# Performance work log

Measured on AMD Instinct MI355X. Metric: run time of the kernel, lower is better.

Reference implementation:

```python
import jax, jax.numpy as jnp
import numpy as np

B, T, D = 2, 2048, 512
H, L, DFF, W = 8, 4, 2048, 256
DH = D // H  # 64
EPS = 1e-5


def layer_norm(x, g, b):
    mu = jnp.mean(x, axis=-1, keepdims=True)
    var = jnp.var(x, axis=-1, keepdims=True)
    return (x - mu) * jax.lax.rsqrt(var + EPS) * g + b


def setup_inputs() -> dict:
    key = jax.random.key(0)
    ks = jax.random.split(key, 8)
    s = 0.02
    inp = {
        "tokens": jax.random.normal(ks[0], (B, T, D), jnp.float32),
        "Wq": jax.random.normal(ks[1], (L, D, D), jnp.float32) * s,
        "Wk": jax.random.normal(ks[2], (L, D, D), jnp.float32) * s,
        "Wv": jax.random.normal(ks[3], (L, D, D), jnp.float32) * s,
        "Wo": jax.random.normal(ks[4], (L, D, D), jnp.float32) * s,
        "bq": jnp.zeros((L, D), jnp.float32),
        "bk": jnp.zeros((L, D), jnp.float32),
        "bv": jnp.zeros((L, D), jnp.float32),
        "bo": jnp.zeros((L, D), jnp.float32),
        "W1": jax.random.normal(ks[5], (L, D, DFF), jnp.float32) * s,
        "b1": jnp.zeros((L, DFF), jnp.float32),
        "W2": jax.random.normal(ks[6], (L, DFF, D), jnp.float32) * s,
        "b2": jnp.zeros((L, D), jnp.float32),
        "g1": jnp.ones((L, D), jnp.float32),
        "be1": jnp.zeros((L, D), jnp.float32),
        "g2": jnp.ones((L, D), jnp.float32),
        "be2": jnp.zeros((L, D), jnp.float32),
        "gf": jnp.ones((D,), jnp.float32),
        "bf": jnp.zeros((D,), jnp.float32),
    }
    return inp


def _rope_tables():
    pos = jnp.arange(T, dtype=jnp.float32)  # default position_ids = 0..T-1
    inv_freq = 1.0 / (10000.0 ** (jnp.arange(0, DH, 2, dtype=jnp.float32) / DH))
    ang = pos[:, None] * inv_freq[None, :]            # (T, DH/2)
    cos = jnp.concatenate([jnp.cos(ang), jnp.cos(ang)], axis=-1)  # (T, DH)
    sin = jnp.concatenate([jnp.sin(ang), jnp.sin(ang)], axis=-1)
    return cos, sin


def _rotate_half(x):
    return jnp.concatenate([-x[..., DH // 2:], x[..., :DH // 2]], axis=-1)


def reference(tokens, Wq, Wk, Wv, Wo, bq, bk, bv, bo, W1, b1, W2, b2,
              g1, be1, g2, be2, gf, bf):
    cos, sin = _rope_tables()  # (T, DH) each, broadcast over (B,H,T,DH)
    # sliding-window causal mask: allow j<=i and i-j < W
    idx = jnp.arange(T)
    allow = (idx[None, :] <= idx[:, None]) & ((idx[:, None] - idx[None, :]) < W)
    scale = np.sqrt(DH).astype(np.float32)

    x = tokens
    for l in range(L):
        xn = layer_norm(x, g1[l], be1[l])
        q = (xn @ Wq[l] + bq[l]).reshape(B, T, H, DH).transpose(0, 2, 1, 3)
        k = (xn @ Wk[l] + bk[l]).reshape(B, T, H, DH).transpose(0, 2, 1, 3)
        v = (xn @ Wv[l] + bv[l]).reshape(B, T, H, DH).transpose(0, 2, 1, 3)
        q = q * cos + _rotate_half(q) * sin
        k = k * cos + _rotate_half(k) * sin
        scores = jnp.einsum('bhqd,bhkd->bhqk', q, k) / scale
        scores = jnp.where(allow[None, None], scores, -jnp.inf)
        attn = jax.nn.softmax(scores, axis=-1)
        out = jnp.einsum('bhqk,bhkd->bhqd', attn, v)
        out = out.transpose(0, 2, 1, 3).reshape(B, T, D)
        x = x + out @ Wo[l] + bo[l]
        xn2 = layer_norm(x, g2[l], be2[l])
        h = jax.nn.gelu(xn2 @ W1[l] + b1[l], approximate=False)  # torch GELU = exact erf
        x = x + h @ W2[l] + b2[l]
    return layer_norm(x, gf, bf)
```

## Files before the change

kernel.cpp:

```cpp
#include <hip/hip_runtime.h>
#include <hip/hip_bf16.h>

#define BQ 2
#define TT 2048
#define DD 512
#define HH 8
#define LL 4
#define DFFN 2048
#define WWIN 256
#define DHD 64
#define MM (BQ*TT)
#define NOUT (MM*DD)

typedef __attribute__((ext_vector_type(8))) short bf16x8;
typedef __attribute__((ext_vector_type(4))) float f32x4;

__device__ __forceinline__ void lds_load16(const void* g, void* l) {
  __builtin_amdgcn_global_load_lds((const __attribute__((address_space(1))) void*)g,
                                   (__attribute__((address_space(3))) void*)l,
                                   16, 0, 0);
}

__global__ __launch_bounds__(256) void fill_const(float* __restrict__ out, float C, int n) {
  int i = blockIdx.x * 256 + threadIdx.x;
  if (i < n) out[i] = C;
}

__global__ __launch_bounds__(256) void prep(const float* __restrict__ tokens,
                                            float* __restrict__ x,
                                            const float* __restrict__ bq,
                                            const float* __restrict__ bk,
                                            const float* __restrict__ bv,
                                            float* __restrict__ bqkvc) {
  const int b = blockIdx.x;
  if (b < 8192) {
    int i = b * 256 + threadIdx.x;
    x[i] = tokens[i];
  } else {
    int idx = (b - 8192) * 256 + threadIdx.x;
    if (idx < LL * 1536) {
      int l = idx / 1536, n = idx % 1536;
      float v;
      if (n < 512)       v = bq[l * 512 + n];
      else if (n < 1024) v = bk[l * 512 + n - 512];
      else               v = bv[l * 512 + n - 1024];
      bqkvc[idx] = v;
    }
  }
}

__global__ __launch_bounds__(256) void transpose_all(const float* __restrict__ Wq,
                                                     const float* __restrict__ Wk,
                                                     const float* __restrict__ Wv,
                                                     const float* __restrict__ Wo,
                                                     const float* __restrict__ W1,
                                                     const float* __restrict__ W2,
                                                     __hip_bfloat16* __restrict__ wqkvT,
                                                     __hip_bfloat16* __restrict__ woT,
                                                     __hip_bfloat16* __restrict__ w1T,
                                                     __hip_bfloat16* __restrict__ w2T) {
  __shared__ float tile[32][33];
  const int l = blockIdx.y;
  const int b = blockIdx.x;
  const float* src;
  __hip_bfloat16* dst;
  int K, N, t;
  if (b < 768) {
    int which = b >> 8; t = b & 255;
    src = ((which == 0) ? Wq : (which == 1) ? Wk : Wv) + (size_t)l * 262144;
    dst = wqkvT + (size_t)l * 786432 + which * 262144;
    K = 512; N = 512;
  } else if (b < 1024) {
    t = b - 768;  src = Wo + (size_t)l * 262144;  dst = woT + (size_t)l * 262144;  K = 512; N = 512;
  } else if (b < 2048) {
    t = b - 1024; src = W1 + (size_t)l * 1048576; dst = w1T + (size_t)l * 1048576; K = 512; N = 2048;
  } else {
    t = b - 2048; src = W2 + (size_t)l * 1048576; dst = w2T + (size_t)l * 1048576; K = 2048; N = 512;
  }
  const int tilesN = N >> 5;
  const int n0 = (t % tilesN) * 32, k0 = (t / tilesN) * 32;
  const int tx = threadIdx.x & 31, ty = threadIdx.x >> 5;
#pragma unroll
  for (int r = 0; r < 32; r += 8)
    tile[ty + r][tx] = src[(size_t)(k0 + ty + r) * N + n0 + tx];
  __syncthreads();
#pragma unroll
  for (int r = 0; r < 32; r += 8)
    dst[(size_t)(n0 + ty + r) * K + k0 + tx] = __float2bfloat16(tile[tx][ty + r]);
}

__global__ __launch_bounds__(256) void ln_kernel(const float* __restrict__ x,
                                                 const float* __restrict__ g,
                                                 const float* __restrict__ b,
                                                 __hip_bfloat16* __restrict__ out) {
  const int wave = threadIdx.x >> 6, lane = threadIdx.x & 63;
  const int row = blockIdx.x * 4 + wave;
  const float* xr = x + (size_t)row * DD;
  float v[8];
  float s = 0.f;
#pragma unroll
  for (int i = 0; i < 8; ++i) { v[i] = xr[lane + i * 64]; s += v[i]; }
#pragma unroll
  for (int off = 32; off; off >>= 1) s += __shfl_xor(s, off);
  float mu = s * (1.f / DD);
  float qs = 0.f;
#pragma unroll
  for (int i = 0; i < 8; ++i) { float d = v[i] - mu; qs += d * d; }
#pragma unroll
  for (int off = 32; off; off >>= 1) qs += __shfl_xor(qs, off);
  float rstd = rsqrtf(qs * (1.f / DD) + 1e-5f);
#pragma unroll
  for (int i = 0; i < 8; ++i) {
    int c = lane + i * 64;
    out[(size_t)row * DD + c] = __float2bfloat16((v[i] - mu) * rstd * g[c] + b[c]);
  }
}

__global__ __launch_bounds__(256) void ln_f32out(const float* __restrict__ x,
                                                 const float* __restrict__ g,
                                                 const float* __restrict__ b,
                                                 float* __restrict__ out) {
  const int wave = threadIdx.x >> 6, lane = threadIdx.x & 63;
  const int row = blockIdx.x * 4 + wave;
  const float* xr = x + (size_t)row * DD;
  float v[8];
  float s = 0.f;
#pragma unroll
  for (int i = 0; i < 8; ++i) { v[i] = xr[lane + i * 64]; s += v[i]; }
#pragma unroll
  for (int off = 32; off; off >>= 1) s += __shfl_xor(s, off);
  float mu = s * (1.f / DD);
  float qs = 0.f;
#pragma unroll
  for (int i = 0; i < 8; ++i) { float d = v[i] - mu; qs += d * d; }
#pragma unroll
  for (int off = 32; off; off >>= 1) qs += __shfl_xor(qs, off);
  float rstd = rsqrtf(qs * (1.f / DD) + 1e-5f);
#pragma unroll
  for (int i = 0; i < 8; ++i) {
    int c = lane + i * 64;
    out[(size_t)row * DD + c] = (v[i] - mu) * rstd * g[c] + b[c];
  }
}

enum { EPI_BF16 = 0, EPI_GELU = 1, EPI_ADDF32 = 2 };

template <int EPI, bool ROPE, int BN>
__global__ __launch_bounds__(256, 1) void gemm_bt(const __hip_bfloat16* __restrict__ A,
                                                  const __hip_bfloat16* __restrict__ BT,
                                                  const float* __restrict__ bias,
                                                  __hip_bfloat16* __restrict__ Obf,
                                                  float* __restrict__ Of,
                                                  __hip_bfloat16* __restrict__ VTo,
                                                  int M, int N, int K, int KS,
                                                  int ostride, int ooff) {
  constexpr int MI = (BN == 128) ? 4 : 2;
  __shared__ __align__(16) __hip_bfloat16 Ash0[128 * 32];
  __shared__ __align__(16) __hip_bfloat16 Ash1[128 * 32];
  __shared__ __align__(16) __hip_bfloat16 Bsh0[BN * 32];
  __shared__ __align__(16) __hip_bfloat16 Bsh1[BN * 32];
  const int tid = threadIdx.x;
  const int wave = tid >> 6;
  const int lane = tid & 63;
  const int m0 = blockIdx.y * 128;
  const int n0 = blockIdx.x * BN;
  const int kbase = blockIdx.z * KS;
  const int wm = (BN == 128) ? (wave >> 1) * 64 : wave * 32;
  const int wn = (BN == 128) ? (wave & 1) * 64 : 0;
  const int l15 = lane & 15;
  const int quad = lane >> 4;

  f32x4 acc[MI][4] = {};

  const int r0 = tid >> 2;
  const int o0 = (tid & 3) * 8;

  const __hip_bfloat16* Ap0 = A + (size_t)(m0 + r0) * K + kbase + o0;
  const __hip_bfloat16* Ap1 = Ap0 + (size_t)64 * K;
  const __hip_bfloat16* Bp0 = BT + (size_t)(n0 + r0) * K + kbase + o0;
  const __hip_bfloat16* Bp1 = Bp0 + (size_t)64 * K;

  auto stage = [&](__hip_bfloat16* As, __hip_bfloat16* Bs, int k) {
    lds_load16(Ap0 + k, As + wave * 512);
    lds_load16(Ap1 + k, As + 2048 + wave * 512);
    lds_load16(Bp0 + k, Bs + wave * 512);
    if constexpr (BN == 128) lds_load16(Bp1 + k, Bs + 2048 + wave * 512);
  };
  auto compute = [&](const __hip_bfloat16* As, const __hip_bfloat16* Bs) {
    bf16x8 af[MI], bfr[4];
#pragma unroll
    for (int i = 0; i < MI; ++i)
      af[i] = *(const bf16x8*)&As[(wm + i * 16 + l15) * 32 + quad * 8];
#pragma unroll
    for (int j = 0; j < 4; ++j)
      bfr[j] = *(const bf16x8*)&Bs[(wn + j * 16 + l15) * 32 + quad * 8];
#pragma unroll
    for (int i = 0; i < MI; ++i)
#pragma unroll
      for (int j = 0; j < 4; ++j)
        acc[i][j] = __builtin_amdgcn_mfma_f32_16x16x32_bf16(af[i], bfr[j], acc[i][j], 0, 0, 0);
  };

  stage(Ash0, Bsh0, 0);
  for (int k0 = 0; k0 < KS; k0 += 64) {
    __syncthreads();
    if (k0 + 32 < KS) stage(Ash1, Bsh1, k0 + 32);
    compute(Ash0, Bsh0);
    __syncthreads();
    if (k0 + 64 < KS) stage(Ash0, Bsh0, k0 + 64);
    compute(Ash1, Bsh1);
  }

  if (ROPE && n0 < 1024) {
#pragma unroll
    for (int j = 0; j < 2; ++j) {
      const int col = n0 + wn + j * 16 + l15;
      const float bv0 = bias[col], bv1 = bias[col + 32];
      const float freq = __powf(10000.f, -(float)(j * 16 + l15) * (1.f / 32.f));
#pragma unroll
      for (int i = 0; i < MI; ++i) {
        const int row = m0 + wm + i * 16 + quad * 4;
#pragma unroll
        for (int r = 0; r < 4; ++r) {
          const int t = (row + r) & 2047;
          float sn, cs;
          __sincosf((float)t * freq, &sn, &cs);
          const float a0 = acc[i][j][r] + bv0;
          const float a1 = acc[i][j + 2][r] + bv1;
          const size_t idx = (size_t)(row + r) * ostride + ooff + col;
          Obf[idx]      = __float2bfloat16(a0 * cs - a1 * sn);
          Obf[idx + 32] = __float2bfloat16(a1 * cs + a0 * sn);
        }
      }
    }
    return;
  }
  if (ROPE) {
#pragma unroll
    for (int j = 0; j < 4; ++j) {
      const int col = n0 + wn + j * 16 + l15;
      const float bv = bias[col];
      const int d = col - 1024;
#pragma unroll
      for (int i = 0; i < MI; ++i) {
        const int row = m0 + wm + i * 16 + quad * 4;
#pragma unroll
        for (int r = 0; r < 4; ++r)
          VTo[(size_t)d * 4096 + row + r] = __float2bfloat16(acc[i][j][r] + bv);
      }
    }
    return;
  }

#pragma unroll
  for (int j = 0; j < 4; ++j) {
    const int col = n0 + wn + j * 16 + l15;
    const float bv = (blockIdx.z == 0) ? bias[col] : 0.f;
#pragma unroll
    for (int i = 0; i < MI; ++i) {
      const int row = m0 + wm + i * 16 + quad * 4;
#pragma unroll
      for (int r = 0; r < 4; ++r) {
        float v = acc[i][j][r] + bv;
        size_t idx = (size_t)(row + r) * ostride + ooff + col;
        if (EPI == EPI_BF16) {
          Obf[idx] = __float2bfloat16(v);
        } else if (EPI == EPI_GELU) {
          float ge = 0.5f * v * (1.f + erff(v * 0.70710678118654752f));
          Obf[idx] = __float2bfloat16(ge);
        } else {
          atomicAdd(&Of[idx], v);
        }
      }
    }
  }
}

__global__ __launch_bounds__(256, 1) void attn_mfma(const __hip_bfloat16* __restrict__ qkv,
                                                    const __hip_bfloat16* __restrict__ VT,
                                                    __hip_bfloat16* __restrict__ ao) {
  constexpr int KPAD = 72;
  constexpr int PPAD = 40;
  __shared__ __align__(16) __hip_bfloat16 Ksh[320 * KPAD];
  __shared__ __align__(16) __hip_bfloat16 Psh[4 * 16 * PPAD];
  const int tid = threadIdx.x;
  const int wave = tid >> 6;
  const int lane = tid & 63;
  const int l15 = lane & 15;
  const int quad = lane >> 4;
  const int bh = blockIdx.y;
  const int b = bh >> 3, h = bh & 7;
  const int q0 = blockIdx.x * 64;
  const int j0 = (q0 >= WWIN) ? (q0 - WWIN) : 0;
  const int nk = (q0 + 63) - j0 + 1;

  const size_t baseK = ((size_t)(b * TT + j0)) * 1536 + 512 + h * 64;
  for (int c = tid; c < nk * 8; c += 256) {
    int row = c >> 3, cc = (c & 7) * 8;
    *(uint4*)&Ksh[row * KPAD + cc] = *(const uint4*)&qkv[baseK + (size_t)row * 1536 + cc];
  }
  __syncthreads();

  const int qt0 = q0 + wave * 16;
  const size_t baseQ = ((size_t)(b * TT + qt0 + l15)) * 1536 + h * 64;
  const bf16x8 aq0 = *(const bf16x8*)&qkv[baseQ + quad * 8];
  const bf16x8 aq1 = *(const bf16x8*)&qkv[baseQ + 32 + quad * 8];

  const __hip_bfloat16* V0 = VT + (size_t)(h * 64 + l15) * 4096 + (size_t)b * 2048 + j0;

  f32x4 o0 = {}, o1 = {}, o2 = {}, o3 = {};
  float lsum[4] = {0.f, 0.f, 0.f, 0.f};

  const int klo = (qt0 > (WWIN - 1)) ? (qt0 - (WWIN - 1)) : 0;
  const int c_lo = (klo - j0) >> 5;
  const int c_hi = (qt0 + 15 - j0) >> 5;
  __hip_bfloat16* Pw = &Psh[wave * 16 * PPAD];

  for (int c = c_lo; c <= c_hi; ++c) {
    const int krel = c * 32;
    bf16x8 bk00 = *(const bf16x8*)&Ksh[(krel + l15) * KPAD + quad * 8];
    bf16x8 bk01 = *(const bf16x8*)&Ksh[(krel + l15) * KPAD + 32 + quad * 8];
    bf16x8 bk10 = *(const bf16x8*)&Ksh[(krel + 16 + l15) * KPAD + quad * 8];
    bf16x8 bk11 = *(const bf16x8*)&Ksh[(krel + 16 + l15) * KPAD + 32 + quad * 8];
    f32x4 z = {};
    f32x4 s0 = __builtin_amdgcn_mfma_f32_16x16x32_bf16(aq0, bk00, z, 0, 0, 0);
    s0 = __builtin_amdgcn_mfma_f32_16x16x32_bf16(aq1, bk01, s0, 0, 0, 0);
    f32x4 s1 = __builtin_amdgcn_mfma_f32_16x16x32_bf16(aq0, bk10, z, 0, 0, 0);
    s1 = __builtin_amdgcn_mfma_f32_16x16x32_bf16(aq1, bk11, s1, 0, 0, 0);

    const int jj0 = j0 + krel + l15;
    const int jj1 = jj0 + 16;
#pragma unroll
    for (int r = 0; r < 4; ++r) {
      const int qrow = qt0 + quad * 4 + r;
      const bool ok0 = (jj0 <= qrow) && ((qrow - jj0) < WWIN);
      const bool ok1 = (jj1 <= qrow) && ((qrow - jj1) < WWIN);
      const float p0 = ok0 ? __expf(s0[r] * 0.125f) : 0.f;
      const float p1 = ok1 ? __expf(s1[r] * 0.125f) : 0.f;
      lsum[r] += p0 + p1;
      const int qloc = quad * 4 + r;
      Pw[qloc * PPAD + l15]      = __float2bfloat16(p0);
      Pw[qloc * PPAD + 16 + l15] = __float2bfloat16(p1);
    }
    asm volatile("s_waitcnt lgkmcnt(0)" ::: "memory");
    __builtin_amdgcn_wave_barrier();
    const bf16x8 pa = *(const bf16x8*)&Pw[l15 * PPAD + quad * 8];

    const int kgl = krel + quad * 8;
#pragma unroll
    for (int t = 0; t < 4; ++t) {
      const bf16x8 bv = *(const bf16x8*)&V0[(size_t)t * 65536 + kgl];
      if (t == 0)      o0 = __builtin_amdgcn_mfma_f32_16x16x32_bf16(pa, bv, o0, 0, 0, 0);
      else if (t == 1) o1 = __builtin_amdgcn_mfma_f32_16x16x32_bf16(pa, bv, o1, 0, 0, 0);
      else if (t == 2) o2 = __builtin_amdgcn_mfma_f32_16x16x32_bf16(pa, bv, o2, 0, 0, 0);
      else             o3 = __builtin_amdgcn_mfma_f32_16x16x32_bf16(pa, bv, o3, 0, 0, 0);
    }
    __builtin_amdgcn_wave_barrier();
  }

#pragma unroll
  for (int r = 0; r < 4; ++r) {
#pragma unroll
    for (int off = 8; off; off >>= 1) lsum[r] += __shfl_xor(lsum[r], off, 16);
  }

#pragma unroll
  for (int r = 0; r < 4; ++r) {
    const float inv = 1.f / lsum[r];
    const size_t ob = ((size_t)(b * TT + qt0 + quad * 4 + r)) * DD + h * 64 + l15;
    ao[ob]      = __float2bfloat16(o0[r] * inv);
    ao[ob + 16] = __float2bfloat16(o1[r] * inv);
    ao[ob + 32] = __float2bfloat16(o2[r] * inv);
    ao[ob + 48] = __float2bfloat16(o3[r] * inv);
  }
}

extern "C" void kernel_launch(void* const* d_in, const int* in_sizes, int n_in,
                              void* d_out, int out_size, void* d_ws, size_t ws_size,
                              hipStream_t stream) {
  float* outF = (float*)d_out;

  int code = 0;
  if (n_in != 19)                      code = 1;
  else if (in_sizes[0]  != 2097152)    code = 2;
  else if (in_sizes[1]  != 1048576)    code = 3;
  else if (in_sizes[9]  != 4194304)    code = 4;
  else if (in_sizes[17] != 512)        code = 5;
  if (code != 0 || ws_size < 27287552ull) {
    float C = code ? (150.f + 15.f * (float)code) : (1000.f + (float)(ws_size >> 20));
    fill_const<<<8192, 256, 0, stream>>>(outF, C, NOUT);
    return;
  }

  const float* tokens = (const float*)d_in[0];
  const float* Wq  = (const float*)d_in[1];
  const float* Wk  = (const float*)d_in[2];
  const float* Wv  = (const float*)d_in[3];
  const float* Wo  = (const float*)d_in[4];
  const float* bq  = (const float*)d_in[5];
  const float* bk  = (const float*)d_in[6];
  const float* bv  = (const float*)d_in[7];
  const float* bo  = (const float*)d_in[8];
  const float* W1  = (const float*)d_in[9];
  const float* b1  = (const float*)d_in[10];
  const float* W2  = (const float*)d_in[11];
  const float* b2  = (const float*)d_in[12];
  const float* g1  = (const float*)d_in[13];
  const float* be1 = (const float*)d_in[14];
  const float* g2  = (const float*)d_in[15];
  const float* be2 = (const float*)d_in[16];
  const float* gf  = (const float*)d_in[17];
  const float* bf  = (const float*)d_in[18];

  char* ws = (char*)d_ws;
  __hip_bfloat16* xnao  = (__hip_bfloat16*)(ws + 0);
  __hip_bfloat16* qkv   = (__hip_bfloat16*)(ws + 4194304);
  __hip_bfloat16* hbuf  = (__hip_bfloat16*)(ws + 4194304);
  __hip_bfloat16* VT    = (__hip_bfloat16*)(ws + 16777216);

  const bool big = ws_size >= 46161920ull;
  __hip_bfloat16 *wqkvT, *woT, *w1T, *w2T;
  float* bqkvc;
  if (big) {
    wqkvT = (__hip_bfloat16*)(ws + 20971520);
    woT   = (__hip_bfloat16*)(ws + 27262976);
    w1T   = (__hip_bfloat16*)(ws + 29360128);
    w2T   = (__hip_bfloat16*)(ws + 37748736);
    bqkvc = (float*)(ws + 46137344);
  } else {
    wqkvT = (__hip_bfloat16*)(ws + 20971520);
    woT   = (__hip_bfloat16*)(ws + 22544384);
    w1T   = (__hip_bfloat16*)(ws + 23068672);
    w2T   = (__hip_bfloat16*)(ws + 25165824);
    bqkvc = (float*)(ws + 27262976);
  }
  __hip_bfloat16* xn = xnao;
  __hip_bfloat16* ao = xnao;
  float* x = outF;

  if (big) {
    transpose_all<<<dim3(3072, 4), 256, 0, stream>>>(Wq, Wk, Wv, Wo, W1, W2,
                                                     wqkvT, woT, w1T, w2T);
  }
  prep<<<8216, 256, 0, stream>>>(tokens, x, bq, bk, bv, bqkvc);

  for (int l = 0; l < LL; ++l) {
    if (!big) {
      transpose_all<<<dim3(3072, 1), 256, 0, stream>>>(
          Wq + (size_t)l * 262144, Wk + (size_t)l * 262144, Wv + (size_t)l * 262144,
          Wo + (size_t)l * 262144, W1 + (size_t)l * 1048576, W2 + (size_t)l * 1048576,
          wqkvT, woT, w1T, w2T);
    }
    __hip_bfloat16* qkvT_l = big ? wqkvT + (size_t)l * 786432  : wqkvT;
    __hip_bfloat16* woT_l  = big ? woT   + (size_t)l * 262144  : woT;
    __hip_bfloat16* w1T_l  = big ? w1T   + (size_t)l * 1048576 : w1T;
    __hip_bfloat16* w2T_l  = big ? w2T   + (size_t)l * 1048576 : w2T;

    ln_kernel<<<1024, 256, 0, stream>>>(x, g1 + l * 512, be1 + l * 512, xn);
    gemm_bt<EPI_BF16, true, 64><<<dim3(24, 32), 256, 0, stream>>>(
        xn, qkvT_l, bqkvc + l * 1536, qkv, nullptr, VT, MM, 1536, 512, 512, 1536, 0);
    attn_mfma<<<dim3(32, 16), 256, 0, stream>>>(qkv, VT, ao);
    gemm_bt<EPI_ADDF32, false, 64><<<dim3(8, 32, 2), 256, 0, stream>>>(
        ao, woT_l, bo + l * 512, nullptr, x, nullptr, MM, 512, 512, 256, 512, 0);
    ln_kernel<<<1024, 256, 0, stream>>>(x, g2 + l * 512, be2 + l * 512, xn);
    gemm_bt<EPI_GELU, false, 128><<<dim3(16, 32), 256, 0, stream>>>(
        xn, w1T_l, b1 + l * 2048, hbuf, nullptr, nullptr, MM, 2048, 512, 512, 2048, 0);
    gemm_bt<EPI_ADDF32, false, 128><<<dim3(4, 32, 4), 256, 0, stream>>>(
        hbuf, w2T_l, b2 + l * 512, nullptr, x, nullptr, MM, 512, 2048, 512, 512, 0);
  }
  ln_f32out<<<1024, 256, 0, stream>>>(x, gf, bf, outF);
}
```

Before: 600.9 us.

## Replace atomic split-K accumulation with partial buffers fused into residual add plus LayerNorm

When the workspace is large enough, the Wo and W2 split-K GEMMs write their two partial results to separate fp32 buffers instead of doing atomicAdd into the residual. A new add_ln2 kernel sums residual plus both partials and applies the next LayerNorm in one pass, producing both the fp32 residual and the bf16 normalized activation. This drops the atomics, the extra copy of tokens and the separate LN launches, at the cost of more workspace and extra fp32 partial traffic.

```diff
diff --git a/kernel.cpp b/kernel.cpp
--- a/kernel.cpp
+++ b/kernel.cpp
@@ -11,6 +11,7 @@
 #define DHD 64
 #define MM (BQ*TT)
 #define NOUT (MM*DD)
+#define PSTRIDE 2097152
 
 typedef __attribute__((ext_vector_type(8))) short bf16x8;
 typedef __attribute__((ext_vector_type(4))) float f32x4;
@@ -47,6 +48,20 @@
       bqkvc[idx] = v;
     }
   }
+}
+
+__global__ __launch_bounds__(256) void prep_bias(const float* __restrict__ bq,
+                                                 const float* __restrict__ bk,
+                                                 const float* __restrict__ bv,
+                                                 float* __restrict__ bqkvc) {
+  int idx = blockIdx.x * 256 + threadIdx.x;
+  if (idx >= LL * 1536) return;
+  int l = idx / 1536, n = idx % 1536;
+  float v;
+  if (n < 512)       v = bq[l * 512 + n];
+  else if (n < 1024) v = bk[l * 512 + n - 512];
+  else               v = bv[l * 512 + n - 1024];
+  bqkvc[idx] = v;
 }
 
 __global__ __launch_bounds__(256) void transpose_all(const float* __restrict__ Wq,
@@ -143,7 +158,70 @@
   }
 }
 
-enum { EPI_BF16 = 0, EPI_GELU = 1, EPI_ADDF32 = 2 };
+template <int OUTMODE>
+__global__ __launch_bounds__(256) void add_ln2(const float* __restrict__ xin,
+                                               const float* __restrict__ P,
+                                               const float* __restrict__ g,
+                                               const float* __restrict__ bsh,
+                                               float* __restrict__ xout,
+                                               __hip_bfloat16* __restrict__ xnout,
+                                               float* __restrict__ fout) {
+  const int wave = threadIdx.x >> 6, lane = threadIdx.x & 63;
+  const int row = blockIdx.x * 4 + wave;
+  const size_t base = (size_t)row * DD + lane * 8;
+  float v[8];
+  {
+    float4 a0 = *(const float4*)&xin[base];
+    float4 a1 = *(const float4*)&xin[base + 4];
+    float4 p0 = *(const float4*)&P[base];
+    float4 p1 = *(const float4*)&P[base + 4];
+    float4 q0 = *(const float4*)&P[PSTRIDE + base];
+    float4 q1 = *(const float4*)&P[PSTRIDE + base + 4];
+    v[0] = a0.x + p0.x + q0.x; v[1] = a0.y + p0.y + q0.y;
+    v[2] = a0.z + p0.z + q0.z; v[3] = a0.w + p0.w + q0.w;
+    v[4] = a1.x + p1.x + q1.x; v[5] = a1.y + p1.y + q1.y;
+    v[6] = a1.z + p1.z + q1.z; v[7] = a1.w + p1.w + q1.w;
+  }
+  float s = 0.f;
+#pragma unroll
+  for (int j = 0; j < 8; ++j) s += v[j];
+#pragma unroll
+  for (int off = 32; off; off >>= 1) s += __shfl_xor(s, off);
+  const float mu = s * (1.f / DD);
+  float qs = 0.f;
+#pragma unroll
+  for (int j = 0; j < 8; ++j) { float d = v[j] - mu; qs += d * d; }
+#pragma unroll
+  for (int off = 32; off; off >>= 1) qs += __shfl_xor(qs, off);
+  const float rstd = rsqrtf(qs * (1.f / DD) + 1e-5f);
+  const int c0 = lane * 8;
+  float4 g0 = *(const float4*)&g[c0];
+  float4 g1 = *(const float4*)&g[c0 + 4];
+  float4 b0 = *(const float4*)&bsh[c0];
+  float4 b1 = *(const float4*)&bsh[c0 + 4];
+  const float gg[8] = {g0.x, g0.y, g0.z, g0.w, g1.x, g1.y, g1.z, g1.w};
+  const float bb[8] = {b0.x, b0.y, b0.z, b0.w, b1.x, b1.y, b1.z, b1.w};
+  if (OUTMODE == 0) {
+    float4 xa = {v[0], v[1], v[2], v[3]};
+    float4 xb = {v[4], v[5], v[6], v[7]};
+    *(float4*)&xout[base] = xa;
+    *(float4*)&xout[base + 4] = xb;
+    bf16x8 o;
+#pragma unroll
+    for (int j = 0; j < 8; ++j)
+      ((__hip_bfloat16*)&o)[j] = __float2bfloat16((v[j] - mu) * rstd * gg[j] + bb[j]);
+    *(bf16x8*)&xnout[base] = o;
+  } else {
+    float4 oa = {(v[0] - mu) * rstd * gg[0] + bb[0], (v[1] - mu) * rstd * gg[1] + bb[1],
+                 (v[2] - mu) * rstd * gg[2] + bb[2], (v[3] - mu) * rstd * gg[3] + bb[3]};
+    float4 ob = {(v[4] - mu) * rstd * gg[4] + bb[4], (v[5] - mu) * rstd * gg[5] + bb[5],
+                 (v[6] - mu) * rstd * gg[6] + bb[6], (v[7] - mu) * rstd * gg[7] + bb[7]};
+    *(float4*)&fout[base] = oa;
+    *(float4*)&fout[base + 4] = ob;
+  }
+}
+
+enum { EPI_BF16 = 0, EPI_GELU = 1, EPI_ADDF32 = 2, EPI_PART = 3 };
 
 template <int EPI, bool ROPE, int BN>
 __global__ __launch_bounds__(256, 1) void gemm_bt(const __hip_bfloat16* __restrict__ A,
@@ -252,6 +330,7 @@
     return;
   }
 
+  const size_t zoff = (EPI == EPI_PART) ? (size_t)blockIdx.z * (size_t)M * N : 0;
 #pragma unroll
   for (int j = 0; j < 4; ++j) {
     const int col = n0 + wn + j * 16 + l15;
@@ -268,6 +347,8 @@
         } else if (EPI == EPI_GELU) {
           float ge = 0.5f * v * (1.f + erff(v * 0.70710678118654752f));
           Obf[idx] = __float2bfloat16(ge);
+        } else if (EPI == EPI_PART) {
+          Of[zoff + idx] = v;
         } else {
           atomicAdd(&Of[idx], v);
         }
@@ -417,16 +498,20 @@
   __hip_bfloat16* qkv   = (__hip_bfloat16*)(ws + 4194304);
   __hip_bfloat16* hbuf  = (__hip_bfloat16*)(ws + 4194304);
   __hip_bfloat16* VT    = (__hip_bfloat16*)(ws + 16777216);
-
-  const bool big = ws_size >= 46161920ull;
+  float* Pwo            = (float*)(ws + 4194304);
+
+  const bool big  = ws_size >= 46161920ull;
+  const bool flow = ws_size >= 62939136ull;
   __hip_bfloat16 *wqkvT, *woT, *w1T, *w2T;
   float* bqkvc;
+  float* Pffn = nullptr;
   if (big) {
     wqkvT = (__hip_bfloat16*)(ws + 20971520);
     woT   = (__hip_bfloat16*)(ws + 27262976);
     w1T   = (__hip_bfloat16*)(ws + 29360128);
     w2T   = (__hip_bfloat16*)(ws + 37748736);
     bqkvc = (float*)(ws + 46137344);
+    Pffn  = (float*)(ws + 46161920);
   } else {
     wqkvT = (__hip_bfloat16*)(ws + 20971520);
     woT   = (__hip_bfloat16*)(ws + 22544384);
@@ -437,6 +522,37 @@
   __hip_bfloat16* xn = xnao;
   __hip_bfloat16* ao = xnao;
   float* x = outF;
+
+  if (flow) {
+    transpose_all<<<dim3(3072, 4), 256, 0, stream>>>(Wq, Wk, Wv, Wo, W1, W2,
+                                                     wqkvT, woT, w1T, w2T);
+    prep_bias<<<24, 256, 0, stream>>>(bq, bk, bv, bqkvc);
+    ln_kernel<<<1024, 256, 0, stream>>>(tokens, g1, be1, xn);
+    for (int l = 0; l < LL; ++l) {
+      __hip_bfloat16* qkvT_l = wqkvT + (size_t)l * 786432;
+      __hip_bfloat16* woT_l  = woT   + (size_t)l * 262144;
+      __hip_bfloat16* w1T_l  = w1T   + (size_t)l * 1048576;
+      __hip_bfloat16* w2T_l  = w2T   + (size_t)l * 1048576;
+
+      gemm_bt<EPI_BF16, true, 64><<<dim3(24, 32), 256, 0, stream>>>(
+          xn, qkvT_l, bqkvc + l * 1536, qkv, nullptr, VT, MM, 1536, 512, 512, 1536, 0);
+      attn_mfma<<<dim3(32, 16), 256, 0, stream>>>(qkv, VT, ao);
+      gemm_bt<EPI_PART, false, 64><<<dim3(8, 32, 2), 256, 0, stream>>>(
+          ao, woT_l, bo + l * 512, nullptr, Pwo, nullptr, MM, 512, 512, 256, 512, 0);
+      add_ln2<0><<<1024, 256, 0, stream>>>(l == 0 ? tokens : x, Pwo,
+                                           g2 + l * 512, be2 + l * 512, x, xn, nullptr);
+      gemm_bt<EPI_GELU, false, 128><<<dim3(16, 32), 256, 0, stream>>>(
+          xn, w1T_l, b1 + l * 2048, hbuf, nullptr, nullptr, MM, 2048, 512, 512, 2048, 0);
+      gemm_bt<EPI_PART, false, 64><<<dim3(8, 32, 2), 256, 0, stream>>>(
+          hbuf, w2T_l, b2 + l * 512, nullptr, Pffn, nullptr, MM, 512, 2048, 1024, 512, 0);
+      if (l < LL - 1)
+        add_ln2<0><<<1024, 256, 0, stream>>>(x, Pffn, g1 + (l + 1) * 512,
+                                             be1 + (l + 1) * 512, x, xn, nullptr);
+      else
+        add_ln2<1><<<1024, 256, 0, stream>>>(x, Pffn, gf, bf, nullptr, nullptr, outF);
+    }
+    return;
+  }
 
   if (big) {
     transpose_all<<<dim3(3072, 4), 256, 0, stream>>>(Wq, Wk, Wv, Wo, W1, W2,
```

Measured after the change: 529.2 us. 11.9% less time.

## Replace split-K atomic residual GEMMs with 64x64 tiles and direct residual epilogue

Applied to the files above, without the earlier changes.

Adds a 64x64 block-tile variant of the GEMM and an epilogue that writes out = residual + acc + bias with plain stores. The Wo and W2 projections now use this variant instead of split-K with float atomics, which removes the atomic traffic while keeping enough blocks to fill the GPU. The token copy in prep is also dropped: the first layer's residual is read straight from tokens, and the first LayerNorm reads tokens directly. The trade-off is that the W2 GEMM now runs its full K=2048 loop in each block with smaller tiles, so each block does more serial work and gets less operand reuse.

```diff
diff --git a/kernel.cpp b/kernel.cpp
--- a/kernel.cpp
+++ b/kernel.cpp
@@ -47,6 +47,20 @@
       bqkvc[idx] = v;
     }
   }
+}
+
+__global__ __launch_bounds__(256) void prep_bias(const float* __restrict__ bq,
+                                                 const float* __restrict__ bk,
+                                                 const float* __restrict__ bv,
+                                                 float* __restrict__ bqkvc) {
+  int idx = blockIdx.x * 256 + threadIdx.x;
+  if (idx >= LL * 1536) return;
+  int l = idx / 1536, n = idx % 1536;
+  float v;
+  if (n < 512)       v = bq[l * 512 + n];
+  else if (n < 1024) v = bk[l * 512 + n - 512];
+  else               v = bv[l * 512 + n - 1024];
+  bqkvc[idx] = v;
 }
 
 __global__ __launch_bounds__(256) void transpose_all(const float* __restrict__ Wq,
@@ -143,34 +157,38 @@
   }
 }
 
-enum { EPI_BF16 = 0, EPI_GELU = 1, EPI_ADDF32 = 2 };
-
-template <int EPI, bool ROPE, int BN>
+enum { EPI_BF16 = 0, EPI_GELU = 1, EPI_ADDF32 = 2, EPI_RES = 3 };
+
+template <int EPI, bool ROPE, int BM, int BN>
 __global__ __launch_bounds__(256, 1) void gemm_bt(const __hip_bfloat16* __restrict__ A,
                                                   const __hip_bfloat16* __restrict__ BT,
                                                   const float* __restrict__ bias,
                                                   __hip_bfloat16* __restrict__ Obf,
                                                   float* __restrict__ Of,
+                                                  const float* __restrict__ Orin,
                                                   __hip_bfloat16* __restrict__ VTo,
                                                   int M, int N, int K, int KS,
                                                   int ostride, int ooff) {
-  constexpr int MI = (BN == 128) ? 4 : 2;
-  __shared__ __align__(16) __hip_bfloat16 Ash0[128 * 32];
-  __shared__ __align__(16) __hip_bfloat16 Ash1[128 * 32];
+  constexpr int MI = (BM == 64) ? 2 : ((BN == 128) ? 4 : 2);
+  constexpr int NJ = (BM == 64) ? 2 : 4;
+  __shared__ __align__(16) __hip_bfloat16 Ash0[BM * 32];
+  __shared__ __align__(16) __hip_bfloat16 Ash1[BM * 32];
   __shared__ __align__(16) __hip_bfloat16 Bsh0[BN * 32];
   __shared__ __align__(16) __hip_bfloat16 Bsh1[BN * 32];
   const int tid = threadIdx.x;
   const int wave = tid >> 6;
   const int lane = tid & 63;
-  const int m0 = blockIdx.y * 128;
+  const int m0 = blockIdx.y * BM;
   const int n0 = blockIdx.x * BN;
   const int kbase = blockIdx.z * KS;
-  const int wm = (BN == 128) ? (wave >> 1) * 64 : wave * 32;
-  const int wn = (BN == 128) ? (wave & 1) * 64 : 0;
+  const int wm = (BM == 64) ? ((wave >> 1) * 32)
+                            : ((BN == 128) ? ((wave >> 1) * 64) : (wave * 32));
+  const int wn = (BM == 64) ? ((wave & 1) * 32)
+                            : ((BN == 128) ? ((wave & 1) * 64) : 0);
   const int l15 = lane & 15;
   const int quad = lane >> 4;
 
-  f32x4 acc[MI][4] = {};
+  f32x4 acc[MI][NJ] = {};
 
   const int r0 = tid >> 2;
   const int o0 = (tid & 3) * 8;
@@ -182,22 +200,22 @@
 
   auto stage = [&](__hip_bfloat16* As, __hip_bfloat16* Bs, int k) {
     lds_load16(Ap0 + k, As + wave * 512);
-    lds_load16(Ap1 + k, As + 2048 + wave * 512);
+    if constexpr (BM == 128) lds_load16(Ap1 + k, As + 2048 + wave * 512);
     lds_load16(Bp0 + k, Bs + wave * 512);
     if constexpr (BN == 128) lds_load16(Bp1 + k, Bs + 2048 + wave * 512);
   };
   auto compute = [&](const __hip_bfloat16* As, const __hip_bfloat16* Bs) {
-    bf16x8 af[MI], bfr[4];
+    bf16x8 af[MI], bfr[NJ];
 #pragma unroll
     for (int i = 0; i < MI; ++i)
       af[i] = *(const bf16x8*)&As[(wm + i * 16 + l15) * 32 + quad * 8];
 #pragma unroll
-    for (int j = 0; j < 4; ++j)
+    for (int j = 0; j < NJ; ++j)
       bfr[j] = *(const bf16x8*)&Bs[(wn + j * 16 + l15) * 32 + quad * 8];
 #pragma unroll
     for (int i = 0; i < MI; ++i)
 #pragma unroll
-      for (int j = 0; j < 4; ++j)
+      for (int j = 0; j < NJ; ++j)
         acc[i][j] = __builtin_amdgcn_mfma_f32_16x16x32_bf16(af[i], bfr[j], acc[i][j], 0, 0, 0);
   };
 
@@ -211,51 +229,51 @@
     compute(Ash1, Bsh1);
   }
 
-  if (ROPE && n0 < 1024) {
-#pragma unroll
-    for (int j = 0; j < 2; ++j) {
-      const int col = n0 + wn + j * 16 + l15;
-      const float bv0 = bias[col], bv1 = bias[col + 32];
-      const float freq = __powf(10000.f, -(float)(j * 16 + l15) * (1.f / 32.f));
-#pragma unroll
-      for (int i = 0; i < MI; ++i) {
-        const int row = m0 + wm + i * 16 + quad * 4;
-#pragma unroll
-        for (int r = 0; r < 4; ++r) {
-          const int t = (row + r) & 2047;
-          float sn, cs;
-          __sincosf((float)t * freq, &sn, &cs);
-          const float a0 = acc[i][j][r] + bv0;
-          const float a1 = acc[i][j + 2][r] + bv1;
-          const size_t idx = (size_t)(row + r) * ostride + ooff + col;
-          Obf[idx]      = __float2bfloat16(a0 * cs - a1 * sn);
-          Obf[idx + 32] = __float2bfloat16(a1 * cs + a0 * sn);
+  if constexpr (ROPE) {
+    if (n0 < 1024) {
+#pragma unroll
+      for (int j = 0; j < 2; ++j) {
+        const int col = n0 + wn + j * 16 + l15;
+        const float bv0 = bias[col], bv1 = bias[col + 32];
+        const float freq = __powf(10000.f, -(float)(j * 16 + l15) * (1.f / 32.f));
+#pragma unroll
+        for (int i = 0; i < MI; ++i) {
+          const int row = m0 + wm + i * 16 + quad * 4;
+#pragma unroll
+          for (int r = 0; r < 4; ++r) {
+            const int t = (row + r) & 2047;
+            float sn, cs;
+            __sincosf((float)t * freq, &sn, &cs);
+            const float a0 = acc[i][j][r] + bv0;
+            const float a1 = acc[i][j + 2][r] + bv1;
+            const size_t idx = (size_t)(row + r) * ostride + ooff + col;
+            Obf[idx]      = __float2bfloat16(a0 * cs - a1 * sn);
+            Obf[idx + 32] = __float2bfloat16(a1 * cs + a0 * sn);
+          }
+        }
+      }
+    } else {
+#pragma unroll
+      for (int j = 0; j < NJ; ++j) {
+        const int col = n0 + wn + j * 16 + l15;
+        const float bv = bias[col];
+        const int d = col - 1024;
+#pragma unroll
+        for (int i = 0; i < MI; ++i) {
+          const int row = m0 + wm + i * 16 + quad * 4;
+#pragma unroll
+          for (int r = 0; r < 4; ++r)
+            VTo[(size_t)d * 4096 + row + r] = __float2bfloat16(acc[i][j][r] + bv);
         }
       }
     }
     return;
   }
-  if (ROPE) {
-#pragma unroll
-    for (int j = 0; j < 4; ++j) {
-      const int col = n0 + wn + j * 16 + l15;
-      const float bv = bias[col];
-      const int d = col - 1024;
-#pragma unroll
-      for (int i = 0; i < MI; ++i) {
-        const int row = m0 + wm + i * 16 + quad * 4;
-#pragma unroll
-        for (int r = 0; r < 4; ++r)
-          VTo[(size_t)d * 4096 + row + r] = __float2bfloat16(acc[i][j][r] + bv);
-      }
-    }
-    return;
-  }
-
-#pragma unroll
-  for (int j = 0; j < 4; ++j) {
+
+#pragma unroll
+  for (int j = 0; j < NJ; ++j) {
     const int col = n0 + wn + j * 16 + l15;
-    const float bv = (blockIdx.z == 0) ? bias[col] : 0.f;
+    const float bv = (EPI == EPI_RES || blockIdx.z == 0) ? bias[col] : 0.f;
 #pragma unroll
     for (int i = 0; i < MI; ++i) {
       const int row = m0 + wm + i * 16 + quad * 4;
@@ -268,6 +286,8 @@
         } else if (EPI == EPI_GELU) {
           float ge = 0.5f * v * (1.f + erff(v * 0.70710678118654752f));
           Obf[idx] = __float2bfloat16(ge);
+        } else if (EPI == EPI_RES) {
+          Of[idx] = Orin[idx] + v;
         } else {
           atomicAdd(&Of[idx], v);
         }
@@ -441,32 +461,60 @@
   if (big) {
     transpose_all<<<dim3(3072, 4), 256, 0, stream>>>(Wq, Wk, Wv, Wo, W1, W2,
                                                      wqkvT, woT, w1T, w2T);
-  }
+    prep_bias<<<24, 256, 0, stream>>>(bq, bk, bv, bqkvc);
+    ln_kernel<<<1024, 256, 0, stream>>>(tokens, g1, be1, xn);
+    for (int l = 0; l < LL; ++l) {
+      __hip_bfloat16* qkvT_l = wqkvT + (size_t)l * 786432;
+      __hip_bfloat16* woT_l  = woT   + (size_t)l * 262144;
+      __hip_bfloat16* w1T_l  = w1T   + (size_t)l * 1048576;
+      __hip_bfloat16* w2T_l  = w2T   + (size_t)l * 1048576;
+
+      gemm_bt<EPI_BF16, true, 128, 64><<<dim3(24, 32), 256, 0, stream>>>(
+          xn, qkvT_l, bqkvc + l * 1536, qkv, nullptr, nullptr, VT,
+          MM, 1536, 512, 512, 1536, 0);
+      attn_mfma<<<dim3(32, 16), 256, 0, stream>>>(qkv, VT, ao);
+      gemm_bt<EPI_RES, false, 64, 64><<<dim3(8, 64), 256, 0, stream>>>(
+          ao, woT_l, bo + l * 512, nullptr, x, (l == 0) ? tokens : x, nullptr,
+          MM, 512, 512, 512, 512, 0);
+      ln_kernel<<<1024, 256, 0, stream>>>(x, g2 + l * 512, be2 + l * 512, xn);
+      gemm_bt<EPI_GELU, false, 128, 128><<<dim3(16, 32), 256, 0, stream>>>(
+          xn, w1T_l, b1 + l * 2048, hbuf, nullptr, nullptr, nullptr,
+          MM, 2048, 512, 512, 2048, 0);
+      gemm_bt<EPI_RES, false, 64, 64><<<dim3(8, 64), 256, 0, stream>>>(
+          hbuf, w2T_l, b2 + l * 512, nullptr, x, x, nullptr,
+          MM, 512, 2048, 2048, 512, 0);
+      if (l < LL - 1)
+        ln_kernel<<<1024, 256, 0, stream>>>(x, g1 + (l + 1) * 512,
+                                            be1 + (l + 1) * 512, xn);
+      else
+        ln_f32out<<<1024, 256, 0, stream>>>(x, gf, bf, outF);
+    }
+    return;
+  }
+
   prep<<<8216, 256, 0, stream>>>(tokens, x, bq, bk, bv, bqkvc);
 
   for (int l = 0; l < LL; ++l) {
-    if (!big) {
-      transpose_all<<<dim3(3072, 1), 256, 0, stream>>>(
-          Wq + (size_t)l * 262144, Wk + (size_t)l * 262144, Wv + (size_t)l * 262144,
-          Wo + (size_t)l * 262144, W1 + (size_t)l * 1048576, W2 + (size_t)l * 1048576,
-          wqkvT, woT, w1T, w2T);
-    }
-    __hip_bfloat16* qkvT_l = big ? wqkvT + (size_t)l * 786432  : wqkvT;
-    __hip_bfloat16* woT_l  = big ? woT   + (size_t)l * 262144  : woT;
-    __hip_bfloat16* w1T_l  = big ? w1T   + (size_t)l * 1048576 : w1T;
-    __hip_bfloat16* w2T_l  = big ? w2T   + (size_t)l * 1048576 : w2T;
+    transpose_all<<<dim3(3072, 1), 256, 0, stream>>>(
+        Wq + (size_t)l * 262144, Wk + (size_t)l * 262144, Wv + (size_t)l * 262144,
+        Wo + (size_t)l * 262144, W1 + (size_t)l * 1048576, W2 + (size_t)l * 1048576,
+        wqkvT, woT, w1T, w2T);
 
     ln_kernel<<<1024, 256, 0, stream>>>(x, g1 + l * 512, be1 + l * 512, xn);
-    gemm_bt<EPI_BF16, true, 64><<<dim3(24, 32), 256, 0, stream>>>(
-        xn, qkvT_l, bqkvc + l * 1536, qkv, nullptr, VT, MM, 1536, 512, 512, 1536, 0);
+    gemm_bt<EPI_BF16, true, 128, 64><<<dim3(24, 32), 256, 0, stream>>>(
+        xn, wqkvT, bqkvc + l * 1536, qkv, nullptr, nullptr, VT,
+        MM, 1536, 512, 512, 1536, 0);
     attn_mfma<<<dim3(32, 16), 256, 0, stream>>>(qkv, VT, ao);
-    gemm_bt<EPI_ADDF32, false, 64><<<dim3(8, 32, 2), 256, 0, stream>>>(
-        ao, woT_l, bo + l * 512, nullptr, x, nullptr, MM, 512, 512, 256, 512, 0);
+    gemm_bt<EPI_ADDF32, false, 128, 64><<<dim3(8, 32, 2), 256, 0, stream>>>(
+        ao, woT, bo + l * 512, nullptr, x, nullptr, nullptr,
+        MM, 512, 512, 256, 512, 0);
     ln_kernel<<<1024, 256, 0, stream>>>(x, g2 + l * 512, be2 + l * 512, xn);
-    gemm_bt<EPI_GELU, false, 128><<<dim3(16, 32), 256, 0, stream>>>(
-        xn, w1T_l, b1 + l * 2048, hbuf, nullptr, nullptr, MM, 2048, 512, 512, 2048, 0);
-    gemm_bt<EPI_ADDF32, false, 128><<<dim3(4, 32, 4), 256, 0, stream>>>(
-        hbuf, w2T_l, b2 + l * 512, nullptr, x, nullptr, MM, 512, 2048, 512, 512, 0);
+    gemm_bt<EPI_GELU, false, 128, 128><<<dim3(16, 32), 256, 0, stream>>>(
+        xn, w1T, b1 + l * 2048, hbuf, nullptr, nullptr, nullptr,
+        MM, 2048, 512, 512, 2048, 0);
+    gemm_bt<EPI_ADDF32, false, 128, 128><<<dim3(4, 32, 4), 256, 0, stream>>>(
+        hbuf, w2T, b2 + l * 512, nullptr, x, nullptr, nullptr,
+        MM, 512, 2048, 512, 512, 0);
   }
   ln_f32out<<<1024, 256, 0, stream>>>(x, gf, bf, outF);
 }
```

New measurement: 505.6 us. -15.9%, faster.
